# Performance work log

Measured on AMD Instinct MI355X. Metric: run time of the kernel, lower is better.

Reference implementation:

```python
import jax, jax.numpy as jnp
import numpy as np

TAU = 2.0
SCALE = 0.125
EPS = 1e-5
HEADS = 8
ALPHA = 4.0  # spikingjelly sigmoid surrogate default

@jax.custom_vjp
def spike(x):
    return (x >= 0.0).astype(x.dtype)

def _spike_fwd(x):
    return spike(x), x

def _spike_bwd(x, g):
    s = jax.nn.sigmoid(ALPHA * x)
    return (g * ALPHA * s * (1.0 - s),)

spike.defvjp(_spike_fwd, _spike_bwd)

def lif(x_seq, vth):
    # MultiStepLIFNode: v += (x - v)/tau; spike = H(v - vth); hard reset to 0 (detach_reset)
    def step(v, x):
        v = v + (x - v) / TAU
        s = spike(v - vth)
        v = v * (1.0 - jax.lax.stop_gradient(s))
        return v, s
    _, s = jax.lax.scan(step, jnp.zeros_like(x_seq[0]), x_seq)
    return s

def bn(y, g, b, m, v):
    # BatchNorm1d in eval form over channel axis 2 of [T,B,C,N]
    shp = (1, 1, -1, 1)
    return (y - m.reshape(shp)) * (g.reshape(shp) / jnp.sqrt(v.reshape(shp) + EPS)) + b.reshape(shp)

def setup_inputs() -> dict:
    key = jax.random.key(0)
    T, B, C, H, W = 4, 32, 512, 16, 16
    ks = jax.random.split(key, 32)
    inp = {"x": jax.random.normal(ks[0], (T, B, C, H, W), jnp.float32)}
    i = 1
    for p in ("q", "k", "v"):
        inp[p + "_w"] = jax.random.normal(ks[i], (C, C), jnp.float32) / np.float32(np.sqrt(C)); i += 1
        inp[p + "_g"] = jax.random.uniform(ks[i], (C,), jnp.float32, 0.5, 1.5); i += 1
        inp[p + "_b"] = jax.random.normal(ks[i], (C,), jnp.float32) * 0.1; i += 1
        inp[p + "_m"] = jax.random.normal(ks[i], (C,), jnp.float32) * 0.1; i += 1
        inp[p + "_v"] = jax.random.uniform(ks[i], (C,), jnp.float32, 0.5, 1.5); i += 1
    inp["p_w"] = jax.random.normal(ks[i], (C, C), jnp.float32) / np.float32(np.sqrt(C)); i += 1
    inp["p_bias"] = jax.random.normal(ks[i], (C,), jnp.float32) * 0.1; i += 1
    inp["p_g"] = jax.random.uniform(ks[i], (C,), jnp.float32, 0.5, 1.5); i += 1
    inp["p_b"] = jax.random.normal(ks[i], (C,), jnp.float32) * 0.1; i += 1
    inp["p_m"] = jax.random.normal(ks[i], (C,), jnp.float32) * 0.1; i += 1
    inp["p_v"] = jax.random.uniform(ks[i], (C,), jnp.float32, 0.5, 1.5); i += 1
    return inp

def reference(x, q_w, q_g, q_b, q_m, q_v, k_w, k_g, k_b, k_m, k_v,
              v_w, v_g, v_b, v_m, v_v, p_w, p_bias, p_g, p_b, p_m, p_v):
    T, B, C, H, W = x.shape
    N = H * W
    h = HEADS
    d = C // h
    xs = lif(x, 1.0).reshape(T, B, C, N)  # proj_lif + flatten(3)

    def branch(w_, g_, b_, m_, var_):
        y = jnp.einsum('oc,tbcn->tbon', w_, xs)  # 1x1 conv1d
        return lif(bn(y, g_, b_, m_, var_), 1.0)

    q = branch(q_w, q_g, q_b, q_m, q_v)
    k = branch(k_w, k_g, k_b, k_m, k_v)
    v = branch(v_w, v_g, v_b, v_m, v_v)
    # [T,B,C,N] -> [T,B,h,N,d]
    def heads(z):
        return z.reshape(T, B, h, d, N).transpose(0, 1, 2, 4, 3)
    q, k, v = heads(q), heads(k), heads(v)
    kv = jnp.einsum('tbhnd,tbhne->tbhde', k, v)  # k^T @ v : [d,d] per head
    a = jnp.einsum('tbhnd,tbhde->tbhne', q, kv) * SCALE
    a = a.transpose(0, 1, 2, 4, 3).reshape(T, B, C, N)
    s = lif(a, 0.5)  # attn_lif, v_threshold=0.5
    y = jnp.einsum('oc,tbcn->tbon', p_w, s) + p_bias.reshape(1, 1, -1, 1)
    y = bn(y, p_g, p_b, p_m, p_v)
    return y.reshape(T, B, C, H, W)
```

## Files before the change

### kernel.cpp

```cpp
#include <hip/hip_runtime.h>
#include <hip/hip_bf16.h>
#include <stdint.h>

#define T_ 4
#define B_ 32
#define C_ 512
#define N_ 256
#define HEADS_ 8

typedef __attribute__((ext_vector_type(8))) short bf16x8;
typedef __attribute__((ext_vector_type(4))) float float4_;
typedef __attribute__((ext_vector_type(16))) float f32x16;

__device__ __forceinline__ unsigned short f2bf(float x){
  unsigned int u = __float_as_uint(x);
  u += 0x7FFFu + ((u >> 16) & 1u);
  return (unsigned short)(u >> 16);
}
__device__ __forceinline__ float bf2f(unsigned short b){
  return __uint_as_float(((unsigned int)b) << 16);
}

__device__ __forceinline__ void gload16(const void* g, void* l){
  __builtin_amdgcn_global_load_lds(
      (const __attribute__((address_space(1))) unsigned int*)g,
      (__attribute__((address_space(3))) unsigned int*)l, 16, 0, 0);
}

__device__ __forceinline__ bf16x8 lds_frag(const unsigned short* base, int row, int cb){
  return *(const bf16x8*)((const char*)base + row * 128 + (cb ^ ((row & 7) << 4)));
}

struct PrepArgs {
  const float* w[4];
  const float* g[4];
  const float* bb[4];
  const float* m[4];
  const float* v[4];
  const float* pbias;
};

__global__ __launch_bounds__(256) void prep_kernel(PrepArgs pa,
    unsigned short* __restrict__ whi, unsigned short* __restrict__ wmid,
    unsigned short* __restrict__ wlo, float* __restrict__ biasv)
{
  int idx = blockIdx.x * 256 + threadIdx.x;
  int mat = idx >> 18;
  int rem = idx & 0x3FFFF;
  int o = rem >> 9;
  float g   = pa.g[mat][o];
  float var = pa.v[mat][o];
  float mm  = pa.m[mat][o];
  float bof = pa.bb[mat][o];
  float rs  = g / sqrtf(var + 1e-5f);
  float wv  = pa.w[mat][rem] * rs;
  unsigned short hi = f2bf(wv);
  float r1 = wv - bf2f(hi);
  unsigned short mid = f2bf(r1);
  float r2 = r1 - bf2f(mid);
  unsigned short lo = f2bf(r2);
  whi[idx] = hi;
  wmid[idx] = mid;
  wlo[idx] = lo;
  if ((rem & 511) == 0){
    float bias = (mat < 3) ? (bof - mm * rs) : ((pa.pbias[o] - mm) * rs + bof);
    biasv[mat * 512 + o] = bias;
  }
}

__global__ __launch_bounds__(256) void lif_tr_kernel(const float* __restrict__ x,
                                                     unsigned short* __restrict__ xsT)
{
  __shared__ alignas(16) unsigned short tile[64][66];
  int bid = blockIdx.x;
  int b  = bid & 31;
  int r  = bid >> 5;
  int ct = r & 7;
  int nt = r >> 3;
  int tid = threadIdx.x;
  int col = tid & 63;
  int rq  = tid >> 6;
  float v[16];
#pragma unroll
  for (int i = 0; i < 16; i++) v[i] = 0.0f;
  const float* xb = x + (size_t)b * C_ * N_ + (size_t)ct * 64 * N_ + nt * 64;
  unsigned short* ob = xsT + (size_t)b * N_ * C_ + (size_t)nt * 64 * C_ + ct * 64;
  for (int t = 0; t < T_; t++){
    const float* xt = xb + (size_t)t * B_ * C_ * N_;
#pragma unroll
    for (int i = 0; i < 16; i++){
      int row = i * 4 + rq;
      float xx = xt[(size_t)row * N_ + col];
      float vv = v[i];
      vv = vv + (xx - vv) * 0.5f;
      bool sp = (vv - 1.0f) >= 0.0f;
      tile[row][col] = sp ? 0x3F80 : 0;
      v[i] = sp ? 0.0f : vv;
    }
    __syncthreads();
    unsigned short* ot = ob + (size_t)t * B_ * N_ * C_;
#pragma unroll
    for (int p = 0; p < 2; p++){
      int nrow = p * 32 + (tid >> 3);
      int c0   = (tid & 7) * 8;
      unsigned int w0 = (unsigned int)tile[c0 + 0][nrow] | ((unsigned int)tile[c0 + 1][nrow] << 16);
      unsigned int w1 = (unsigned int)tile[c0 + 2][nrow] | ((unsigned int)tile[c0 + 3][nrow] << 16);
      unsigned int w2 = (unsigned int)tile[c0 + 4][nrow] | ((unsigned int)tile[c0 + 5][nrow] << 16);
      unsigned int w3 = (unsigned int)tile[c0 + 6][nrow] | ((unsigned int)tile[c0 + 7][nrow] << 16);
      uint4 v4{w0, w1, w2, w3};
      *(uint4*)(ot + (size_t)nrow * C_ + c0) = v4;
    }
    __syncthreads();
  }
}

__global__ __launch_bounds__(256, 2) void branch_kernel(
    const unsigned short* __restrict__ whi, const unsigned short* __restrict__ wmid,
    const unsigned short* __restrict__ wlo,
    const float* __restrict__ biasv, const unsigned short* __restrict__ xsT,
    unsigned short* __restrict__ qT, unsigned short* __restrict__ kS,
    unsigned short* __restrict__ vS)
{
  __shared__ alignas(16) unsigned short As[3][64 * 64];
  __shared__ alignas(16) unsigned short Bs[256 * 64];
  __shared__ alignas(16) float bias_lds[64];

  int bid = blockIdx.x;
  int b  = bid & 31;
  int r2 = bid >> 5;
  int ot = r2 & 7;
  int br = r2 >> 3;
  int o0 = ot * 64;
  int tid = threadIdx.x;
  int w    = tid >> 6;
  int lane = tid & 63;
  int lm = lane & 31;
  int hi = lane >> 5;

  if (tid < 64) bias_lds[tid] = biasv[br * 512 + o0 + tid];

  const unsigned short* wsrc[3] = { whi + (size_t)br * 262144,
                                    wmid + (size_t)br * 262144,
                                    wlo + (size_t)br * 262144 };

  f32x16 acc[2][2];
  float  st[2][2][16];
#pragma unroll
  for (int a = 0; a < 2; a++)
#pragma unroll
    for (int c = 0; c < 2; c++)
#pragma unroll
      for (int i = 0; i < 16; i++) st[a][c][i] = 0.0f;

  for (int t = 0; t < T_; t++){
#pragma unroll
    for (int a = 0; a < 2; a++)
#pragma unroll
      for (int c = 0; c < 2; c++)
#pragma unroll
        for (int i = 0; i < 16; i++) acc[a][c][i] = 0.0f;

    const unsigned short* bsrc = xsT + (size_t)(t * B_ + b) * N_ * C_;

    for (int kk = 0; kk < 8; kk++){
      __syncthreads();
#pragma unroll
      for (int term = 0; term < 3; term++){
#pragma unroll
        for (int p = 0; p < 2; p++){
          int chunk = p * 256 + tid;
          int row = chunk >> 3, cb = (chunk & 7) * 16;
          gload16((const char*)(wsrc[term] + (size_t)(o0 + row) * 512 + kk * 64)
                      + (cb ^ ((row & 7) << 4)),
                  (char*)As[term] + chunk * 16);
        }
      }
#pragma unroll
      for (int p = 0; p < 8; p++){
        int chunk = p * 256 + tid;
        int row = chunk >> 3, cb = (chunk & 7) * 16;
        gload16((const char*)(bsrc + (size_t)row * C_ + kk * 64)
                    + (cb ^ ((row & 7) << 4)),
                (char*)Bs + chunk * 16);
      }
      __syncthreads();
#pragma unroll
      for (int ks = 0; ks < 4; ks++){
        int cb = ks * 32 + 16 * hi;
        bf16x8 b0  = lds_frag(Bs, w * 64 + lm,      cb);
        bf16x8 b1  = lds_frag(Bs, w * 64 + 32 + lm, cb);
#pragma unroll
        for (int term = 0; term < 3; term++){
          bf16x8 a0 = lds_frag(As[term], lm,      cb);
          bf16x8 a1 = lds_frag(As[term], 32 + lm, cb);
          acc[0][0] = __builtin_amdgcn_mfma_f32_32x32x16_bf16(a0, b0, acc[0][0], 0, 0, 0);
          acc[0][1] = __builtin_amdgcn_mfma_f32_32x32x16_bf16(a0, b1, acc[0][1], 0, 0, 0);
          acc[1][0] = __builtin_amdgcn_mfma_f32_32x32x16_bf16(a1, b0, acc[1][0], 0, 0, 0);
          acc[1][1] = __builtin_amdgcn_mfma_f32_32x32x16_bf16(a1, b1, acc[1][1], 0, 0, 0);
        }
      }
    }
    __syncthreads();
#pragma unroll
    for (int mf = 0; mf < 2; mf++){
#pragma unroll
      for (int nf = 0; nf < 2; nf++){
        int n_loc = w * 64 + nf * 32 + lm;
#pragma unroll
        for (int rq = 0; rq < 4; rq++){
          float4_ b4 = *(const float4_*)&bias_lds[mf * 32 + 8 * rq + 4 * hi];
          unsigned short sb[4];
#pragma unroll
          for (int rr = 0; rr < 4; rr++){
            int r = rq * 4 + rr;
            float y = acc[mf][nf][r] + b4[rr];
            float vv = st[mf][nf][r];
            vv = vv + (y - vv) * 0.5f;
            bool sp = (vv - 1.0f) >= 0.0f;
            st[mf][nf][r] = sp ? 0.0f : vv;
            sb[rr] = sp ? 0x3F80 : 0;
          }
          if (br == 0){
            unsigned int u0 = (unsigned int)sb[0] | ((unsigned int)sb[1] << 16);
            unsigned int u1 = (unsigned int)sb[2] | ((unsigned int)sb[3] << 16);
            int o0b = (mf * 32 + 8 * rq + 4 * hi) * 2;
            *(unsigned long long*)((char*)Bs + n_loc * 128 + (o0b ^ ((n_loc & 7) << 4)))
                = ((unsigned long long)u1 << 32) | u0;
          } else {
#pragma unroll
            for (int rr = 0; rr < 4; rr++){
              int o_loc = mf * 32 + rr + 8 * rq + 4 * hi;
              *(unsigned short*)((char*)Bs + o_loc * 512 + n_loc * 2) = sb[rr];
            }
          }
        }
      }
    }
    __syncthreads();
    if (br == 0){
      unsigned short* dst = qT + (size_t)(t * B_ + b) * N_ * C_ + o0;
#pragma unroll
      for (int p = 0; p < 8; p++){
        int chunk = p * 256 + tid;
        int row = chunk >> 3, cb = (chunk & 7) * 16;
        uint4 val = *(const uint4*)((const char*)Bs + row * 128 + (cb ^ ((row & 7) << 4)));
        *(uint4*)((char*)dst + (size_t)row * 1024 + cb) = val;
      }
    } else {
      unsigned short* dst = (br == 1 ? kS : vS) + ((size_t)(t * B_ + b) * C_ + o0) * N_;
#pragma unroll
      for (int p = 0; p < 8; p++){
        int chunk = p * 256 + tid;
        int row = chunk >> 5, nb = (chunk & 31) * 16;
        uint4 val = *(const uint4*)((const char*)Bs + row * 512 + nb);
        *(uint4*)((char*)dst + (size_t)row * 512 + nb) = val;
      }
    }
  }
}

__global__ __launch_bounds__(256, 2) void attn_kernel(
    const unsigned short* __restrict__ qT, const unsigned short* __restrict__ kS,
    const unsigned short* __restrict__ vS, unsigned short* __restrict__ sT)
{
  __shared__ alignas(16) unsigned short Ks[64 * 64];
  __shared__ alignas(16) unsigned short Vs[64 * 64];
  __shared__ alignas(16) unsigned short KVT[64 * 64];
  __shared__ alignas(16) unsigned short Qs[256 * 64];

  int bid = blockIdx.x;
  int b = bid & 31;
  int h = bid >> 5;
  int tid = threadIdx.x;
  int w = tid >> 6;
  int lane = tid & 63;
  int lm = lane & 31, hi = lane >> 5;
  int mfk = w >> 1, nfk = w & 1;

  float stA[2][2][16];
#pragma unroll
  for (int a = 0; a < 2; a++)
#pragma unroll
  for (int c = 0; c < 2; c++)
#pragma unroll
  for (int i = 0; i < 16; i++) stA[a][c][i] = 0.0f;

  for (int t = 0; t < T_; t++){
    const unsigned short* ksrc = kS + ((size_t)(t * B_ + b) * C_ + h * 64) * N_;
    const unsigned short* vsrc = vS + ((size_t)(t * B_ + b) * C_ + h * 64) * N_;
    const unsigned short* qsrc = qT + (size_t)(t * B_ + b) * N_ * C_ + h * 64;
    unsigned short* sdst = sT + (size_t)(t * B_ + b) * N_ * C_ + h * 64;

    f32x16 kvacc;
#pragma unroll
    for (int i = 0; i < 16; i++) kvacc[i] = 0.0f;

    for (int ch = 0; ch < 4; ch++){
      __syncthreads();
#pragma unroll
      for (int p = 0; p < 2; p++){
        int chunk = p * 256 + tid;
        int row = chunk >> 3, cb = (chunk & 7) * 16;
        int so = (cb ^ ((row & 7) << 4));
        gload16((const char*)ksrc + (size_t)row * 512 + ch * 128 + so,
                (char*)Ks + chunk * 16);
        gload16((const char*)vsrc + (size_t)row * 512 + ch * 128 + so,
                (char*)Vs + chunk * 16);
      }
      __syncthreads();
#pragma unroll
      for (int ki = 0; ki < 4; ki++){
        int cb = ki * 32 + 16 * hi;
        bf16x8 ak = lds_frag(Ks, mfk * 32 + lm, cb);
        bf16x8 bv = lds_frag(Vs, nfk * 32 + lm, cb);
        kvacc = __builtin_amdgcn_mfma_f32_32x32x16_bf16(ak, bv, kvacc, 0, 0, 0);
      }
    }
    {
      int e = nfk * 32 + lm;
#pragma unroll
      for (int rq = 0; rq < 4; rq++){
        unsigned int u0 = (unsigned int)f2bf(kvacc[rq * 4 + 0])
                        | ((unsigned int)f2bf(kvacc[rq * 4 + 1]) << 16);
        unsigned int u1 = (unsigned int)f2bf(kvacc[rq * 4 + 2])
                        | ((unsigned int)f2bf(kvacc[rq * 4 + 3]) << 16);
        int d0b = (mfk * 32 + 8 * rq + 4 * hi) * 2;
        *(unsigned long long*)((char*)KVT + e * 128 + (d0b ^ ((e & 7) << 4)))
            = ((unsigned long long)u1 << 32) | u0;
      }
    }
#pragma unroll
    for (int p = 0; p < 8; p++){
      int chunk = p * 256 + tid;
      int row = chunk >> 3, cb = (chunk & 7) * 16;
      gload16((const char*)qsrc + (size_t)row * 1024 + (cb ^ ((row & 7) << 4)),
              (char*)Qs + chunk * 16);
    }
    __syncthreads();
    f32x16 aacc[2][2];
#pragma unroll
    for (int a = 0; a < 2; a++)
#pragma unroll
    for (int c = 0; c < 2; c++)
#pragma unroll
    for (int i = 0; i < 16; i++) aacc[a][c][i] = 0.0f;
#pragma unroll
    for (int ki = 0; ki < 4; ki++){
      int cb = ki * 32 + 16 * hi;
      bf16x8 aq0 = lds_frag(Qs, w * 64 + lm,      cb);
      bf16x8 aq1 = lds_frag(Qs, w * 64 + 32 + lm, cb);
      bf16x8 b0  = lds_frag(KVT, lm,      cb);
      bf16x8 b1  = lds_frag(KVT, 32 + lm, cb);
      aacc[0][0] = __builtin_amdgcn_mfma_f32_32x32x16_bf16(aq0, b0, aacc[0][0], 0, 0, 0);
      aacc[0][1] = __builtin_amdgcn_mfma_f32_32x32x16_bf16(aq0, b1, aacc[0][1], 0, 0, 0);
      aacc[1][0] = __builtin_amdgcn_mfma_f32_32x32x16_bf16(aq1, b0, aacc[1][0], 0, 0, 0);
      aacc[1][1] = __builtin_amdgcn_mfma_f32_32x32x16_bf16(aq1, b1, aacc[1][1], 0, 0, 0);
    }
#pragma unroll
    for (int mf = 0; mf < 2; mf++){
#pragma unroll
      for (int nf = 0; nf < 2; nf++){
        int e_loc = nf * 32 + lm;
#pragma unroll
        for (int r = 0; r < 16; r++){
          float aval = aacc[mf][nf][r] * 0.125f;
          float vv = stA[mf][nf][r];
          vv = vv + (aval - vv) * 0.5f;
          bool sp = (vv - 0.5f) >= 0.0f;
          stA[mf][nf][r] = sp ? 0.0f : vv;
          int n_loc = w * 64 + mf * 32 + (r & 3) + 8 * (r >> 2) + 4 * hi;
          *(unsigned short*)((char*)Qs + n_loc * 128 + ((e_loc * 2) ^ ((n_loc & 7) << 4))) = sp ? 0x3F80 : 0;
        }
      }
    }
    __syncthreads();
#pragma unroll
    for (int p = 0; p < 8; p++){
      int chunk = p * 256 + tid;
      int row = chunk >> 3, cb = (chunk & 7) * 16;
      uint4 val = *(const uint4*)((const char*)Qs + row * 128 + (cb ^ ((row & 7) << 4)));
      *(uint4*)((char*)sdst + (size_t)row * 1024 + cb) = val;
    }
  }
}

__global__ __launch_bounds__(256, 2) void proj_kernel(
    const unsigned short* __restrict__ whi, const unsigned short* __restrict__ wmid,
    const unsigned short* __restrict__ wlo,
    const float* __restrict__ biasv, const unsigned short* __restrict__ sT,
    float* __restrict__ out)
{
  __shared__ alignas(16) unsigned short As[3][64 * 64];
  __shared__ alignas(16) unsigned short Bs[256 * 64];
  __shared__ alignas(16) float bias_lds[64];

  int bid = blockIdx.x;
  int tb = bid & 127;
  int ot = bid >> 7;
  int t = tb >> 5, b = tb & 31;
  int o0 = ot * 64;
  int tid = threadIdx.x;
  int w = tid >> 6, lane = tid & 63, lm = lane & 31, hi = lane >> 5;

  if (tid < 64) bias_lds[tid] = biasv[3 * 512 + o0 + tid];

  const unsigned short* wsrc[3] = { whi + (size_t)3 * 262144,
                                    wmid + (size_t)3 * 262144,
                                    wlo + (size_t)3 * 262144 };
  const unsigned short* bsrc = sT + (size_t)(t * B_ + b) * N_ * C_;

  f32x16 acc[2][2];
#pragma unroll
  for (int a = 0; a < 2; a++)
#pragma unroll
    for (int c = 0; c < 2; c++)
#pragma unroll
      for (int i = 0; i < 16; i++) acc[a][c][i] = 0.0f;

  for (int kk = 0; kk < 8; kk++){
    __syncthreads();
#pragma unroll
    for (int term = 0; term < 3; term++){
#pragma unroll
      for (int p = 0; p < 2; p++){
        int chunk = p * 256 + tid;
        int row = chunk >> 3, cb = (chunk & 7) * 16;
        gload16((const char*)(wsrc[term] + (size_t)(o0 + row) * 512 + kk * 64)
                    + (cb ^ ((row & 7) << 4)),
                (char*)As[term] + chunk * 16);
      }
    }
#pragma unroll
    for (int p = 0; p < 8; p++){
      int chunk = p * 256 + tid;
      int row = chunk >> 3, cb = (chunk & 7) * 16;
      gload16((const char*)(bsrc + (size_t)row * C_ + kk * 64)
                  + (cb ^ ((row & 7) << 4)),
              (char*)Bs + chunk * 16);
    }
    __syncthreads();
#pragma unroll
    for (int ks = 0; ks < 4; ks++){
      int cb = ks * 32 + 16 * hi;
      bf16x8 b0  = lds_frag(Bs, w * 64 + lm,      cb);
      bf16x8 b1  = lds_frag(Bs, w * 64 + 32 + lm, cb);
#pragma unroll
      for (int term = 0; term < 3; term++){
        bf16x8 a0 = lds_frag(As[term], lm,      cb);
        bf16x8 a1 = lds_frag(As[term], 32 + lm, cb);
        acc[0][0] = __builtin_amdgcn_mfma_f32_32x32x16_bf16(a0, b0, acc[0][0], 0, 0, 0);
        acc[0][1] = __builtin_amdgcn_mfma_f32_32x32x16_bf16(a0, b1, acc[0][1], 0, 0, 0);
        acc[1][0] = __builtin_amdgcn_mfma_f32_32x32x16_bf16(a1, b0, acc[1][0], 0, 0, 0);
        acc[1][1] = __builtin_amdgcn_mfma_f32_32x32x16_bf16(a1, b1, acc[1][1], 0, 0, 0);
      }
    }
  }
  float* dst = out + ((size_t)(t * B_ + b) * C_ + o0) * N_;
#pragma unroll
  for (int mf = 0; mf < 2; mf++){
#pragma unroll
    for (int nf = 0; nf < 2; nf++){
      int n_loc = w * 64 + nf * 32 + lm;
#pragma unroll
      for (int rq = 0; rq < 4; rq++){
        float4_ b4 = *(const float4_*)&bias_lds[mf * 32 + 8 * rq + 4 * hi];
#pragma unroll
        for (int rr = 0; rr < 4; rr++){
          int o_loc = mf * 32 + rr + 8 * rq + 4 * hi;
          dst[(size_t)o_loc * N_ + n_loc] = acc[mf][nf][rq * 4 + rr] + b4[rr];
        }
      }
    }
  }
}

extern "C" void kernel_launch(void* const* d_in, const int* in_sizes, int n_in,
                              void* d_out, int out_size, void* d_ws, size_t ws_size,
                              hipStream_t stream) {
  const float* x = (const float*)d_in[0];
  PrepArgs pa;
  pa.w[0]  = (const float*)d_in[1];
  pa.g[0]  = (const float*)d_in[2];
  pa.bb[0] = (const float*)d_in[3];
  pa.m[0]  = (const float*)d_in[4];
  pa.v[0]  = (const float*)d_in[5];
  pa.w[1]  = (const float*)d_in[6];
  pa.g[1]  = (const float*)d_in[7];
  pa.bb[1] = (const float*)d_in[8];
  pa.m[1]  = (const float*)d_in[9];
  pa.v[1]  = (const float*)d_in[10];
  pa.w[2]  = (const float*)d_in[11];
  pa.g[2]  = (const float*)d_in[12];
  pa.bb[2] = (const float*)d_in[13];
  pa.m[2]  = (const float*)d_in[14];
  pa.v[2]  = (const float*)d_in[15];
  pa.w[3]  = (const float*)d_in[16];
  pa.pbias = (const float*)d_in[17];
  pa.g[3]  = (const float*)d_in[18];
  pa.bb[3] = (const float*)d_in[19];
  pa.m[3]  = (const float*)d_in[20];
  pa.v[3]  = (const float*)d_in[21];

  char* ws = (char*)d_ws;
  unsigned short* whi  = (unsigned short*)(ws);
  unsigned short* wmid = (unsigned short*)(ws + 0x200000);
  unsigned short* wlo  = (unsigned short*)(ws + 0x400000);
  float*          biasv= (float*)(ws + 0x600000);
  unsigned short* xsT  = (unsigned short*)(ws + 0x610000);
  unsigned short* sTp  = xsT;
  unsigned short* qT   = (unsigned short*)(ws + 0x610000 + (size_t)32*1024*1024);
  unsigned short* kS   = (unsigned short*)(ws + 0x610000 + (size_t)64*1024*1024);
  unsigned short* vS   = (unsigned short*)(ws + 0x610000 + (size_t)96*1024*1024);

  prep_kernel<<<4096, 256, 0, stream>>>(pa, whi, wmid, wlo, biasv);
  lif_tr_kernel<<<1024, 256, 0, stream>>>(x, xsT);
  branch_kernel<<<768, 256, 0, stream>>>(whi, wmid, wlo, biasv, xsT, qT, kS, vS);
  attn_kernel<<<256, 256, 0, stream>>>(qT, kS, vS, sTp);
  proj_kernel<<<1024, 256, 0, stream>>>(whi, wmid, wlo, biasv, sTp, (float*)d_out);
}
```

Baseline: 404.5 us.

## Double-buffer branch and proj GEMM tiles with 512-thread blocks and K=32 stages

Restructures the branch and proj GEMM kernels to use 512 threads (8 waves in a 2x4 grid), halve the K step to 32, and double-buffer the LDS tiles so the loads for the next K slice overlap the MFMA work on the current one. The hi/mid/lo weight terms are now addressed at fixed 1 MiB offsets from whi rather than through separate pointers, which relies on wmid and wlo lying contiguously after whi in the workspace. The intent is to hide global-load latency and raise occupancy. The cost is more barrier iterations and a smaller per-wave tile, which gives less register reuse.

```diff
diff --git a/kernel.cpp b/kernel.cpp
--- a/kernel.cpp
+++ b/kernel.cpp
@@ -27,8 +27,29 @@
       (__attribute__((address_space(3))) unsigned int*)l, 16, 0, 0);
 }
 
-__device__ __forceinline__ bf16x8 lds_frag(const unsigned short* base, int row, int cb){
-  return *(const bf16x8*)((const char*)base + row * 128 + (cb ^ ((row & 7) << 4)));
+__device__ __forceinline__ bf16x8 frag32(const unsigned short* base, int row, int cb){
+  return *(const bf16x8*)((const char*)base + row * 64 + (cb ^ (((row >> 1) & 3) << 4)));
+}
+
+__device__ __forceinline__ void stage_tiles(const unsigned short* wbase,
+    const unsigned short* bsrc, int kk, int tid,
+    unsigned short* Asb, unsigned short* Bsb)
+{
+  { int c = tid; int term = c >> 8; int ct = c & 255; int row = ct >> 2; int slot = ct & 3;
+    const char* s = (const char*)(wbase + (size_t)term * 1048576 + (size_t)row * 512 + kk * 32)
+                    + ((slot * 16) ^ (((row >> 1) & 3) << 4));
+    gload16(s, (char*)Asb + c * 16); }
+  if (tid < 256){
+    int c = 512 + tid; int ct = c & 255; int row = ct >> 2; int slot = ct & 3;
+    const char* s = (const char*)(wbase + (size_t)2 * 1048576 + (size_t)row * 512 + kk * 32)
+                    + ((slot * 16) ^ (((row >> 1) & 3) << 4));
+    gload16(s, (char*)Asb + c * 16); }
+#pragma unroll
+  for (int p = 0; p < 2; p++){
+    int c = p * 512 + tid; int row = c >> 2; int slot = c & 3;
+    const char* s = (const char*)(bsrc + (size_t)row * 512 + kk * 32)
+                    + ((slot * 16) ^ (((row >> 1) & 3) << 4));
+    gload16(s, (char*)Bsb + c * 16); }
 }
 
 struct PrepArgs {
@@ -114,15 +135,14 @@
   }
 }
 
-__global__ __launch_bounds__(256, 2) void branch_kernel(
-    const unsigned short* __restrict__ whi, const unsigned short* __restrict__ wmid,
-    const unsigned short* __restrict__ wlo,
+__global__ __launch_bounds__(512, 4) void branch_kernel(
+    const unsigned short* __restrict__ whi,
     const float* __restrict__ biasv, const unsigned short* __restrict__ xsT,
     unsigned short* __restrict__ qT, unsigned short* __restrict__ kS,
     unsigned short* __restrict__ vS)
 {
-  __shared__ alignas(16) unsigned short As[3][64 * 64];
-  __shared__ alignas(16) unsigned short Bs[256 * 64];
+  __shared__ alignas(16) unsigned short As[2][3 * 2048];
+  __shared__ alignas(16) unsigned short Bs[2][8192];
   __shared__ alignas(16) float bias_lds[64];
 
   int bid = blockIdx.x;
@@ -132,106 +152,85 @@
   int br = r2 >> 3;
   int o0 = ot * 64;
   int tid = threadIdx.x;
-  int w    = tid >> 6;
+  int wv   = tid >> 6;
+  int wr   = wv >> 2;
+  int wc   = wv & 3;
   int lane = tid & 63;
   int lm = lane & 31;
   int hi = lane >> 5;
 
   if (tid < 64) bias_lds[tid] = biasv[br * 512 + o0 + tid];
 
-  const unsigned short* wsrc[3] = { whi + (size_t)br * 262144,
-                                    wmid + (size_t)br * 262144,
-                                    wlo + (size_t)br * 262144 };
-
-  f32x16 acc[2][2];
-  float  st[2][2][16];
-#pragma unroll
-  for (int a = 0; a < 2; a++)
+  const unsigned short* wbase = whi + (size_t)br * 262144 + (size_t)o0 * 512;
+
+  f32x16 acc[2];
+  float  st[2][16];
+#pragma unroll
+  for (int c = 0; c < 2; c++)
+#pragma unroll
+    for (int i = 0; i < 16; i++) st[c][i] = 0.0f;
+
+  for (int t = 0; t < T_; t++){
 #pragma unroll
     for (int c = 0; c < 2; c++)
 #pragma unroll
-      for (int i = 0; i < 16; i++) st[a][c][i] = 0.0f;
-
-  for (int t = 0; t < T_; t++){
-#pragma unroll
-    for (int a = 0; a < 2; a++)
-#pragma unroll
-      for (int c = 0; c < 2; c++)
-#pragma unroll
-        for (int i = 0; i < 16; i++) acc[a][c][i] = 0.0f;
+      for (int i = 0; i < 16; i++) acc[c][i] = 0.0f;
 
     const unsigned short* bsrc = xsT + (size_t)(t * B_ + b) * N_ * C_;
 
-    for (int kk = 0; kk < 8; kk++){
+    stage_tiles(wbase, bsrc, 0, tid, As[0], Bs[0]);
+    __syncthreads();
+
+    for (int kk = 0; kk < 16; kk++){
+      int cur = kk & 1;
+      if (kk < 15) stage_tiles(wbase, bsrc, kk + 1, tid, As[cur ^ 1], Bs[cur ^ 1]);
+#pragma unroll
+      for (int ks = 0; ks < 2; ks++){
+        int cb = ks * 32 + 16 * hi;
+        bf16x8 b0 = frag32(Bs[cur], wc * 64 + lm,      cb);
+        bf16x8 b1 = frag32(Bs[cur], wc * 64 + 32 + lm, cb);
+        bf16x8 a0 = frag32(As[cur] + 0 * 2048, wr * 32 + lm, cb);
+        acc[0] = __builtin_amdgcn_mfma_f32_32x32x16_bf16(a0, b0, acc[0], 0, 0, 0);
+        acc[1] = __builtin_amdgcn_mfma_f32_32x32x16_bf16(a0, b1, acc[1], 0, 0, 0);
+        bf16x8 a1 = frag32(As[cur] + 1 * 2048, wr * 32 + lm, cb);
+        acc[0] = __builtin_amdgcn_mfma_f32_32x32x16_bf16(a1, b0, acc[0], 0, 0, 0);
+        acc[1] = __builtin_amdgcn_mfma_f32_32x32x16_bf16(a1, b1, acc[1], 0, 0, 0);
+        bf16x8 a2 = frag32(As[cur] + 2 * 2048, wr * 32 + lm, cb);
+        acc[0] = __builtin_amdgcn_mfma_f32_32x32x16_bf16(a2, b0, acc[0], 0, 0, 0);
+        acc[1] = __builtin_amdgcn_mfma_f32_32x32x16_bf16(a2, b1, acc[1], 0, 0, 0);
+      }
       __syncthreads();
-#pragma unroll
-      for (int term = 0; term < 3; term++){
-#pragma unroll
-        for (int p = 0; p < 2; p++){
-          int chunk = p * 256 + tid;
-          int row = chunk >> 3, cb = (chunk & 7) * 16;
-          gload16((const char*)(wsrc[term] + (size_t)(o0 + row) * 512 + kk * 64)
-                      + (cb ^ ((row & 7) << 4)),
-                  (char*)As[term] + chunk * 16);
+    }
+
+    unsigned short* bounce = (unsigned short*)Bs;
+#pragma unroll
+    for (int nf = 0; nf < 2; nf++){
+      int n_loc = wc * 64 + nf * 32 + lm;
+#pragma unroll
+      for (int rq = 0; rq < 4; rq++){
+        float4_ b4 = *(const float4_*)&bias_lds[wr * 32 + 8 * rq + 4 * hi];
+        unsigned short sb[4];
+#pragma unroll
+        for (int rr = 0; rr < 4; rr++){
+          int r = rq * 4 + rr;
+          float y = acc[nf][r] + b4[rr];
+          float vvv = st[nf][r];
+          vvv = vvv + (y - vvv) * 0.5f;
+          bool sp = (vvv - 1.0f) >= 0.0f;
+          st[nf][r] = sp ? 0.0f : vvv;
+          sb[rr] = sp ? 0x3F80 : 0;
         }
-      }
-#pragma unroll
-      for (int p = 0; p < 8; p++){
-        int chunk = p * 256 + tid;
-        int row = chunk >> 3, cb = (chunk & 7) * 16;
-        gload16((const char*)(bsrc + (size_t)row * C_ + kk * 64)
-                    + (cb ^ ((row & 7) << 4)),
-                (char*)Bs + chunk * 16);
-      }
-      __syncthreads();
-#pragma unroll
-      for (int ks = 0; ks < 4; ks++){
-        int cb = ks * 32 + 16 * hi;
-        bf16x8 b0  = lds_frag(Bs, w * 64 + lm,      cb);
-        bf16x8 b1  = lds_frag(Bs, w * 64 + 32 + lm, cb);
-#pragma unroll
-        for (int term = 0; term < 3; term++){
-          bf16x8 a0 = lds_frag(As[term], lm,      cb);
-          bf16x8 a1 = lds_frag(As[term], 32 + lm, cb);
-          acc[0][0] = __builtin_amdgcn_mfma_f32_32x32x16_bf16(a0, b0, acc[0][0], 0, 0, 0);
-          acc[0][1] = __builtin_amdgcn_mfma_f32_32x32x16_bf16(a0, b1, acc[0][1], 0, 0, 0);
-          acc[1][0] = __builtin_amdgcn_mfma_f32_32x32x16_bf16(a1, b0, acc[1][0], 0, 0, 0);
-          acc[1][1] = __builtin_amdgcn_mfma_f32_32x32x16_bf16(a1, b1, acc[1][1], 0, 0, 0);
-        }
-      }
-    }
-    __syncthreads();
-#pragma unroll
-    for (int mf = 0; mf < 2; mf++){
-#pragma unroll
-      for (int nf = 0; nf < 2; nf++){
-        int n_loc = w * 64 + nf * 32 + lm;
-#pragma unroll
-        for (int rq = 0; rq < 4; rq++){
-          float4_ b4 = *(const float4_*)&bias_lds[mf * 32 + 8 * rq + 4 * hi];
-          unsigned short sb[4];
+        if (br == 0){
+          unsigned int u0 = (unsigned int)sb[0] | ((unsigned int)sb[1] << 16);
+          unsigned int u1 = (unsigned int)sb[2] | ((unsigned int)sb[3] << 16);
+          int o0b = (wr * 32 + 8 * rq + 4 * hi) * 2;
+          *(unsigned long long*)((char*)bounce + n_loc * 128 + (o0b ^ ((n_loc & 7) << 4)))
+              = ((unsigned long long)u1 << 32) | u0;
+        } else {
 #pragma unroll
           for (int rr = 0; rr < 4; rr++){
-            int r = rq * 4 + rr;
-            float y = acc[mf][nf][r] + b4[rr];
-            float vv = st[mf][nf][r];
-            vv = vv + (y - vv) * 0.5f;
-            bool sp = (vv - 1.0f) >= 0.0f;
-            st[mf][nf][r] = sp ? 0.0f : vv;
-            sb[rr] = sp ? 0x3F80 : 0;
-          }
-          if (br == 0){
-            unsigned int u0 = (unsigned int)sb[0] | ((unsigned int)sb[1] << 16);
-            unsigned int u1 = (unsigned int)sb[2] | ((unsigned int)sb[3] << 16);
-            int o0b = (mf * 32 + 8 * rq + 4 * hi) * 2;
-            *(unsigned long long*)((char*)Bs + n_loc * 128 + (o0b ^ ((n_loc & 7) << 4)))
-                = ((unsigned long long)u1 << 32) | u0;
-          } else {
-#pragma unroll
-            for (int rr = 0; rr < 4; rr++){
-              int o_loc = mf * 32 + rr + 8 * rq + 4 * hi;
-              *(unsigned short*)((char*)Bs + o_loc * 512 + n_loc * 2) = sb[rr];
-            }
+            int o_loc = wr * 32 + rr + 8 * rq + 4 * hi;
+            *(unsigned short*)((char*)bounce + o_loc * 512 + n_loc * 2) = sb[rr];
           }
         }
       }
@@ -240,23 +239,28 @@
     if (br == 0){
       unsigned short* dst = qT + (size_t)(t * B_ + b) * N_ * C_ + o0;
 #pragma unroll
-      for (int p = 0; p < 8; p++){
-        int chunk = p * 256 + tid;
-        int row = chunk >> 3, cb = (chunk & 7) * 16;
-        uint4 val = *(const uint4*)((const char*)Bs + row * 128 + (cb ^ ((row & 7) << 4)));
-        *(uint4*)((char*)dst + (size_t)row * 1024 + cb) = val;
+      for (int p = 0; p < 4; p++){
+        int chunk = p * 512 + tid;
+        int row = chunk >> 3, cbq = (chunk & 7) * 16;
+        uint4 val = *(const uint4*)((const char*)bounce + row * 128 + (cbq ^ ((row & 7) << 4)));
+        *(uint4*)((char*)dst + (size_t)row * 1024 + cbq) = val;
       }
     } else {
       unsigned short* dst = (br == 1 ? kS : vS) + ((size_t)(t * B_ + b) * C_ + o0) * N_;
 #pragma unroll
-      for (int p = 0; p < 8; p++){
-        int chunk = p * 256 + tid;
+      for (int p = 0; p < 4; p++){
+        int chunk = p * 512 + tid;
         int row = chunk >> 5, nb = (chunk & 31) * 16;
-        uint4 val = *(const uint4*)((const char*)Bs + row * 512 + nb);
+        uint4 val = *(const uint4*)((const char*)bounce + row * 512 + nb);
         *(uint4*)((char*)dst + (size_t)row * 512 + nb) = val;
       }
     }
+    __syncthreads();
   }
+}
+
+__device__ __forceinline__ bf16x8 lds_frag(const unsigned short* base, int row, int cb){
+  return *(const bf16x8*)((const char*)base + row * 128 + (cb ^ ((row & 7) << 4)));
 }
 
 __global__ __launch_bounds__(256, 2) void attn_kernel(
@@ -302,10 +306,8 @@
         int chunk = p * 256 + tid;
         int row = chunk >> 3, cb = (chunk & 7) * 16;
         int so = (cb ^ ((row & 7) << 4));
-        gload16((const char*)ksrc + (size_t)row * 512 + ch * 128 + so,
-                (char*)Ks + chunk * 16);
-        gload16((const char*)vsrc + (size_t)row * 512 + ch * 128 + so,
-                (char*)Vs + chunk * 16);
+        gload16((const char*)ksrc + (size_t)row * 512 + ch * 128 + so, (char*)Ks + chunk * 16);
+        gload16((const char*)vsrc + (size_t)row * 512 + ch * 128 + so, (char*)Vs + chunk * 16);
       }
       __syncthreads();
 #pragma unroll
@@ -364,10 +366,10 @@
 #pragma unroll
         for (int r = 0; r < 16; r++){
           float aval = aacc[mf][nf][r] * 0.125f;
-          float vv = stA[mf][nf][r];
-          vv = vv + (aval - vv) * 0.5f;
-          bool sp = (vv - 0.5f) >= 0.0f;
-          stA[mf][nf][r] = sp ? 0.0f : vv;
+          float vvv = stA[mf][nf][r];
+          vvv = vvv + (aval - vvv) * 0.5f;
+          bool sp = (vvv - 0.5f) >= 0.0f;
+          stA[mf][nf][r] = sp ? 0.0f : vvv;
           int n_loc = w * 64 + mf * 32 + (r & 3) + 8 * (r >> 2) + 4 * hi;
           *(unsigned short*)((char*)Qs + n_loc * 128 + ((e_loc * 2) ^ ((n_loc & 7) << 4))) = sp ? 0x3F80 : 0;
         }
@@ -384,14 +386,13 @@
   }
 }
 
-__global__ __launch_bounds__(256, 2) void proj_kernel(
-    const unsigned short* __restrict__ whi, const unsigned short* __restrict__ wmid,
-    const unsigned short* __restrict__ wlo,
+__global__ __launch_bounds__(512, 4) void proj_kernel(
+    const unsigned short* __restrict__ whi,
     const float* __restrict__ biasv, const unsigned short* __restrict__ sT,
     float* __restrict__ out)
 {
-  __shared__ alignas(16) unsigned short As[3][64 * 64];
-  __shared__ alignas(16) unsigned short Bs[256 * 64];
+  __shared__ alignas(16) unsigned short As[2][3 * 2048];
+  __shared__ alignas(16) unsigned short Bs[2][8192];
   __shared__ alignas(16) float bias_lds[64];
 
   int bid = blockIdx.x;
@@ -400,75 +401,55 @@
   int t = tb >> 5, b = tb & 31;
   int o0 = ot * 64;
   int tid = threadIdx.x;
-  int w = tid >> 6, lane = tid & 63, lm = lane & 31, hi = lane >> 5;
+  int wv = tid >> 6, wr = wv >> 2, wc = wv & 3;
+  int lane = tid & 63, lm = lane & 31, hi = lane >> 5;
 
   if (tid < 64) bias_lds[tid] = biasv[3 * 512 + o0 + tid];
 
-  const unsigned short* wsrc[3] = { whi + (size_t)3 * 262144,
-                                    wmid + (size_t)3 * 262144,
-                                    wlo + (size_t)3 * 262144 };
+  const unsigned short* wbase = whi + (size_t)3 * 262144 + (size_t)o0 * 512;
   const unsigned short* bsrc = sT + (size_t)(t * B_ + b) * N_ * C_;
 
-  f32x16 acc[2][2];
-#pragma unroll
-  for (int a = 0; a < 2; a++)
-#pragma unroll
-    for (int c = 0; c < 2; c++)
-#pragma unroll
-      for (int i = 0; i < 16; i++) acc[a][c][i] = 0.0f;
-
-  for (int kk = 0; kk < 8; kk++){
-    __syncthreads();
-#pragma unroll
-    for (int term = 0; term < 3; term++){
-#pragma unroll
-      for (int p = 0; p < 2; p++){
-        int chunk = p * 256 + tid;
-        int row = chunk >> 3, cb = (chunk & 7) * 16;
-        gload16((const char*)(wsrc[term] + (size_t)(o0 + row) * 512 + kk * 64)
-                    + (cb ^ ((row & 7) << 4)),
-                (char*)As[term] + chunk * 16);
-      }
-    }
-#pragma unroll
-    for (int p = 0; p < 8; p++){
-      int chunk = p * 256 + tid;
-      int row = chunk >> 3, cb = (chunk & 7) * 16;
-      gload16((const char*)(bsrc + (size_t)row * C_ + kk * 64)
-                  + (cb ^ ((row & 7) << 4)),
-              (char*)Bs + chunk * 16);
-    }
-    __syncthreads();
-#pragma unroll
-    for (int ks = 0; ks < 4; ks++){
+  f32x16 acc[2];
+#pragma unroll
+  for (int c = 0; c < 2; c++)
+#pragma unroll
+    for (int i = 0; i < 16; i++) acc[c][i] = 0.0f;
+
+  stage_tiles(wbase, bsrc, 0, tid, As[0], Bs[0]);
+  __syncthreads();
+
+  for (int kk = 0; kk < 16; kk++){
+    int cur = kk & 1;
+    if (kk < 15) stage_tiles(wbase, bsrc, kk + 1, tid, As[cur ^ 1], Bs[cur ^ 1]);
+#pragma unroll
+    for (int ks = 0; ks < 2; ks++){
       int cb = ks * 32 + 16 * hi;
-      bf16x8 b0  = lds_frag(Bs, w * 64 + lm,      cb);
-      bf16x8 b1  = lds_frag(Bs, w * 64 + 32 + lm, cb);
-#pragma unroll
-      for (int term = 0; term < 3; term++){
-        bf16x8 a0 = lds_frag(As[term], lm,      cb);
-        bf16x8 a1 = lds_frag(As[term], 32 + lm, cb);
-        acc[0][0] = __builtin_amdgcn_mfma_f32_32x32x16_bf16(a0, b0, acc[0][0], 0, 0, 0);
-        acc[0][1] = __builtin_amdgcn_mfma_f32_32x32x16_bf16(a0, b1, acc[0][1], 0, 0, 0);
-        acc[1][0] = __builtin_amdgcn_mfma_f32_32x32x16_bf16(a1, b0, acc[1][0], 0, 0, 0);
-        acc[1][1] = __builtin_amdgcn_mfma_f32_32x32x16_bf16(a1, b1, acc[1][1], 0, 0, 0);
-      }
-    }
+      bf16x8 b0 = frag32(Bs[cur], wc * 64 + lm,      cb);
+      bf16x8 b1 = frag32(Bs[cur], wc * 64 + 32 + lm, cb);
+      bf16x8 a0 = frag32(As[cur] + 0 * 2048, wr * 32 + lm, cb);
+      acc[0] = __builtin_amdgcn_mfma_f32_32x32x16_bf16(a0, b0, acc[0], 0, 0, 0);
+      acc[1] = __builtin_amdgcn_mfma_f32_32x32x16_bf16(a0, b1, acc[1], 0, 0, 0);
+      bf16x8 a1 = frag32(As[cur] + 1 * 2048, wr * 32 + lm, cb);
+      acc[0] = __builtin_amdgcn_mfma_f32_32x32x16_bf16(a1, b0, acc[0], 0, 0, 0);
+      acc[1] = __builtin_amdgcn_mfma_f32_32x32x16_bf16(a1, b1, acc[1], 0, 0, 0);
+      bf16x8 a2 = frag32(As[cur] + 2 * 2048, wr * 32 + lm, cb);
+      acc[0] = __builtin_amdgcn_mfma_f32_32x32x16_bf16(a2, b0, acc[0], 0, 0, 0);
+      acc[1] = __builtin_amdgcn_mfma_f32_32x32x16_bf16(a2, b1, acc[1], 0, 0, 0);
+    }
+    __syncthreads();
   }
+
   float* dst = out + ((size_t)(t * B_ + b) * C_ + o0) * N_;
 #pragma unroll
-  for (int mf = 0; mf < 2; mf++){
-#pragma unroll
-    for (int nf = 0; nf < 2; nf++){
-      int n_loc = w * 64 + nf * 32 + lm;
-#pragma unroll
-      for (int rq = 0; rq < 4; rq++){
-        float4_ b4 = *(const float4_*)&bias_lds[mf * 32 + 8 * rq + 4 * hi];
-#pragma unroll
-        for (int rr = 0; rr < 4; rr++){
-          int o_loc = mf * 32 + rr + 8 * rq + 4 * hi;
-          dst[(size_t)o_loc * N_ + n_loc] = acc[mf][nf][rq * 4 + rr] + b4[rr];
-        }
+  for (int nf = 0; nf < 2; nf++){
+    int n_loc = wc * 64 + nf * 32 + lm;
+#pragma unroll
+    for (int rq = 0; rq < 4; rq++){
+      float4_ b4 = *(const float4_*)&bias_lds[wr * 32 + 8 * rq + 4 * hi];
+#pragma unroll
+      for (int rr = 0; rr < 4; rr++){
+        int o_loc = wr * 32 + rr + 8 * rq + 4 * hi;
+        dst[(size_t)o_loc * N_ + n_loc] = acc[nf][rq * 4 + rr] + b4[rr];
       }
     }
   }
@@ -514,7 +495,7 @@
 
   prep_kernel<<<4096, 256, 0, stream>>>(pa, whi, wmid, wlo, biasv);
   lif_tr_kernel<<<1024, 256, 0, stream>>>(x, xsT);
-  branch_kernel<<<768, 256, 0, stream>>>(whi, wmid, wlo, biasv, xsT, qT, kS, vS);
+  branch_kernel<<<768, 512, 0, stream>>>(whi, biasv, xsT, qT, kS, vS);
   attn_kernel<<<256, 256, 0, stream>>>(qT, kS, vS, sTp);
-  proj_kernel<<<1024, 256, 0, stream>>>(whi, wmid, wlo, biasv, sTp, (float*)d_out);
-}
+  proj_kernel<<<1024, 512, 0, stream>>>(whi, biasv, sTp, (float*)d_out);
+}
```

Result: slower. 480.6 us (+18.8%).
